# Optimization experiments

Measured on AMD Instinct MI355X. Metric: run time of the kernel, lower is better.

## Reference

```python
import jax, jax.numpy as jnp
import numpy as np

# Forest structure: T_TREES complete trees with branching BR and edge-depth DEPTH.
# Node layout: level-major; within a level, tree-major, siblings consecutive, so the
# parent of the k-th node of level l is the (k // BR)-th node of level l-1.
T_TREES, BR, DEPTH = 128, 2, 11
C, L, M, G = 8, 2, 256, 4  # hidden states, max outdegree, alphabet, n_gen
_sizes = [T_TREES * BR ** l for l in range(DEPTH + 1)]
_offs = np.concatenate([[0], np.cumsum(_sizes)])
DIM = int(_offs[-1])
LEVEL_NODES = [jnp.arange(int(_offs[l]), int(_offs[l + 1])) for l in range(DEPTH + 1)]
LEAVES = LEVEL_NODES[DEPTH]


def setup_inputs():
    key = jax.random.key(0)
    k = jax.random.split(key, 6)
    # batch id of node (level l, within-level idx i) is i // BR**l -> repeat pattern
    batch = jnp.concatenate([jnp.repeat(jnp.arange(T_TREES, dtype=jnp.int32), BR ** l)
                             for l in range(DEPTH + 1)])
    return {
        "lambda_A": jax.random.uniform(k[0], (C, C, L, G), dtype=jnp.float32),
        "lambda_B": jax.random.uniform(k[1], (C, M, G), dtype=jnp.float32),
        "lambda_Pi": jax.random.uniform(k[2], (C, L, G), dtype=jnp.float32),
        "lambda_SP": jax.random.uniform(k[3], (L, G), dtype=jnp.float32),
        "pos": jax.random.randint(k[4], (DIM,), 0, L, dtype=jnp.int32),
        "x": jax.random.randint(k[5], (DIM,), 0, M, dtype=jnp.int32),
        "batch": batch,
    }


def reference(lambda_A, lambda_B, lambda_Pi, lambda_SP, pos, x, batch):
    # Faithful ReversedUpwardDownward.forward ('bu' mode) of HiddenTreeMarkovModel.
    A = jax.nn.softmax(lambda_A, axis=0)    # (C,C,L,G): column-stochastic over parent state
    Bm = jax.nn.softmax(lambda_B, axis=1)   # (C,M,G): emission
    Pi = jax.nn.softmax(lambda_Pi, axis=0)  # (C,L,G): leaf prior per position
    SP = jax.nn.softmax(lambda_SP, axis=0)  # (L,G): switching-parent weights

    beta = jnp.zeros((DIM, C, G), lambda_A.dtype)
    ll = jnp.zeros((DIM, G), lambda_A.dtype)

    # leaves
    beta_lv = (Pi[:, pos[LEAVES]] * Bm[:, x[LEAVES]]).transpose(1, 0, 2)  # (nl,C,G)
    nu = beta_lv.sum(1)                                                   # (nl,G)
    beta = beta.at[LEAVES].set(beta_lv / nu[:, None])
    ll = ll.at[LEAVES].set(jnp.log(nu))

    # bottom-up level recursion
    for l in range(DEPTH, 0, -1):
        ch, pa = LEVEL_NODES[l], LEVEL_NODES[l - 1]
        pos_ch = pos[ch]                                   # (n,)
        # t_beta_ch[n,c,g] = SP[pos_ch] * sum_d A[c,d,pos_ch,g] * beta[ch][d,g]
        msgs = jnp.einsum('cdpg,ndg->ncpg', A, beta[ch])   # (n,C,L,G); avoids (n,C,C,G)
        sel = jax.nn.one_hot(pos_ch, L, dtype=msgs.dtype)  # (n,L)
        t_beta_ch = SP[pos_ch][:, None, :] * jnp.einsum('ncpg,np->ncg', msgs, sel)
        # scatter-add to parents == exact sum over the BR consecutive siblings
        t_beta_pa = t_beta_ch.reshape(pa.shape[0], BR, C, G).sum(1)  # (npa,C,G)
        beta_pa = t_beta_pa * Bm[:, x[pa]].transpose(1, 0, 2)
        nu = beta_pa.sum(1)
        beta = beta.at[pa].set(beta_pa / nu[:, None])
        ll = ll.at[pa].set(jnp.log(nu))

    # per-tree total log-likelihood
    return jax.ops.segment_sum(ll, batch, num_segments=T_TREES)  # (T_TREES, G)
```

## Files before the change

kernel.cpp:

```cpp
#include <hip/hip_runtime.h>
#include <math.h>


#define NTHREADS 1024
#define NSTRIDE 17

__global__ __launch_bounds__(NTHREADS) void htmm_kernel(
    const float* __restrict__ lA,
    const float* __restrict__ lB,
    const float* __restrict__ lPi,
    const float* __restrict__ lSP,
    const int* __restrict__ pos,
    const int* __restrict__ xx,
    float* __restrict__ out)
{
    __shared__ float sBm[16 * 256];
    __shared__ float sA[256];
    __shared__ float sPi[32];
    __shared__ float sSP[4];
    __shared__ float sInv[16];
    __shared__ float buf0[512 * NSTRIDE];
    __shared__ float buf1[256 * NSTRIDE];
    __shared__ double sLL[2];

    const int tid = threadIdx.x;
    const int t  = blockIdx.x >> 1;
    const int g0 = (blockIdx.x & 1) << 1;

    if (tid < 2) sLL[tid] = 0.0;

#pragma unroll
    for (int k = 0; k < 4; ++k) {
        int idx = tid + k * NTHREADS;
        int c = idx >> 9, m = (idx >> 1) & 255, gi = idx & 1;
        sBm[((c << 1) | gi) * 256 + m] = expf(lB[c * 1024 + m * 4 + g0 + gi]);
    }
    __syncthreads();

    if (tid < 256) {
        int r = tid >> 4, seg = tid & 15;
        float s = 0.f;
#pragma unroll
        for (int i = 0; i < 16; ++i) s += sBm[r * 256 + seg * 16 + ((i + seg) & 15)];
#pragma unroll
        for (int o = 8; o >= 1; o >>= 1) s += __shfl_xor(s, o, 64);
        if (seg == 0) sInv[r] = 1.0f / s;
    } else if (tid >= 256 && tid < 288) {
        int w = tid - 256;
        int d = w >> 2, pp = (w >> 1) & 1, gi = w & 1;
        float e[8]; float s = 0.f;
#pragma unroll
        for (int c = 0; c < 8; ++c) { e[c] = expf(lA[c * 64 + d * 8 + pp * 4 + g0 + gi]); s += e[c]; }
        float inv = 1.f / s;
#pragma unroll
        for (int c = 0; c < 8; ++c) sA[(((pp << 1) | gi) * 8 + c) * 8 + d] = e[c] * inv;
    } else if (tid >= 288 && tid < 292) {
        int w = tid - 288; int pp = w >> 1, gi = w & 1;
        float e[8]; float s = 0.f;
#pragma unroll
        for (int c = 0; c < 8; ++c) { e[c] = expf(lPi[c * 8 + pp * 4 + g0 + gi]); s += e[c]; }
        float inv = 1.f / s;
#pragma unroll
        for (int c = 0; c < 8; ++c) sPi[((pp << 1) | gi) * 8 + c] = e[c] * inv;
    } else if (tid >= 292 && tid < 294) {
        int gi = tid - 292;
        float e0 = expf(lSP[g0 + gi]), e1 = expf(lSP[4 + g0 + gi]);
        float inv = 1.f / (e0 + e1);
        sSP[gi] = e0 * inv; sSP[2 + gi] = e1 * inv;
    }
    __syncthreads();

#pragma unroll
    for (int k = 0; k < 4; ++k) {
        int idx = tid + k * NTHREADS;
        sBm[idx] *= sInv[idx >> 8];
    }
    __syncthreads();

    float ll0 = 0.f, ll1 = 0.f;

    {
        const int j  = tid & 511;
        const int gi = tid >> 9;
        const int4 pv4 = *(const int4*)(pos + 262016 + t * 2048 + 4 * j);
        const int4 xv4 = *(const int4*)(xx  + 262016 + t * 2048 + 4 * j);
        const int2 pu2 = *(const int2*)(pos + 130944 + t * 1024 + 2 * j);
        const int2 xu2 = *(const int2*)(xx  + 130944 + t * 1024 + 2 * j);
        const int xq = xx[65408 + t * 512 + j];

        float llacc = 0.f;
        float tq[8] = {0,0,0,0,0,0,0,0};
#pragma unroll
        for (int u = 0; u < 2; ++u) {
            float tu[8] = {0,0,0,0,0,0,0,0};
#pragma unroll
            for (int v = 0; v < 2; ++v) {
                const int k = 2 * u + v;
                const int pv  = (k == 0) ? pv4.x : (k == 1) ? pv4.y : (k == 2) ? pv4.z : pv4.w;
                const int xvv = (k == 0) ? xv4.x : (k == 1) ? xv4.y : (k == 2) ? xv4.z : xv4.w;
                const float* Pip = &sPi[((pv << 1) | gi) << 3];
                float b[8]; float nu = 0.f;
#pragma unroll
                for (int c = 0; c < 8; ++c) {
                    b[c] = Pip[c] * sBm[((c << 1) | gi) * 256 + xvv];
                    nu += b[c];
                }
                llacc += logf(nu);
                const float scale = sSP[(pv << 1) | gi] / nu;
                const float* Ap = &sA[((pv << 1) | gi) << 6];
#pragma unroll
                for (int c = 0; c < 8; ++c) {
                    float s = 0.f;
#pragma unroll
                    for (int d = 0; d < 8; ++d) s += Ap[(c << 3) + d] * b[d];
                    tu[c] += scale * s;
                }
            }
            const int pu = u ? pu2.y : pu2.x;
            const int xu = u ? xu2.y : xu2.x;
            float bu[8]; float nuu = 0.f;
#pragma unroll
            for (int c = 0; c < 8; ++c) { bu[c] = tu[c] * sBm[((c << 1) | gi) * 256 + xu]; nuu += bu[c]; }
            llacc += logf(nuu);
            const float scale = sSP[(pu << 1) | gi] / nuu;
            const float* Ap = &sA[((pu << 1) | gi) << 6];
#pragma unroll
            for (int c = 0; c < 8; ++c) {
                float s = 0.f;
#pragma unroll
                for (int d = 0; d < 8; ++d) s += Ap[(c << 3) + d] * bu[d];
                tq[c] += scale * s;
            }
        }
        float bq[8]; float nuq = 0.f;
#pragma unroll
        for (int c = 0; c < 8; ++c) { bq[c] = tq[c] * sBm[((c << 1) | gi) * 256 + xq]; nuq += bq[c]; }
        llacc += logf(nuq);
        const float inv = 1.f / nuq;
#pragma unroll
        for (int c = 0; c < 8; ++c) buf0[j * NSTRIDE + (gi << 3) + c] = bq[c] * inv;

        if (gi == 0) ll0 += llacc; else ll1 += llacc;
    }
    __syncthreads();

    float* bin = buf0;
    float* bout = buf1;
    for (int l = 9; l >= 1; --l) {
        const int nP = 1 << (l - 1);
        const int nItems = nP << 1;
        const int chBase = 128 * ((1 << l) - 1) + t * (1 << l);
        const int paBase = 128 * (nP - 1) + t * nP;
        if (tid < nItems) {
            const int p  = tid & (nP - 1);
            const int gi = tid >> (l - 1);
            const int2 pch = *(const int2*)(pos + chBase + 2 * p);
            const int xpa = xx[paBase + p];
            float tp[8] = {0,0,0,0,0,0,0,0};
#pragma unroll
            for (int u = 0; u < 2; ++u) {
                const int pw = u ? pch.y : pch.x;
                const float* bip = &bin[(2 * p + u) * NSTRIDE + (gi << 3)];
                float b[8];
#pragma unroll
                for (int d = 0; d < 8; ++d) b[d] = bip[d];
                const float scale = sSP[(pw << 1) | gi];
                const float* Ap = &sA[((pw << 1) | gi) << 6];
#pragma unroll
                for (int c = 0; c < 8; ++c) {
                    float s = 0.f;
#pragma unroll
                    for (int d = 0; d < 8; ++d) s += Ap[(c << 3) + d] * b[d];
                    tp[c] += scale * s;
                }
            }
            float bpv[8]; float nu = 0.f;
#pragma unroll
            for (int c = 0; c < 8; ++c) { bpv[c] = tp[c] * sBm[((c << 1) | gi) * 256 + xpa]; nu += bpv[c]; }
            const float llv = logf(nu);
            const float inv = 1.f / nu;
#pragma unroll
            for (int c = 0; c < 8; ++c) bout[p * NSTRIDE + (gi << 3) + c] = bpv[c] * inv;
            if (gi == 0) ll0 += llv; else ll1 += llv;
        }
        __syncthreads();
        float* tmpp = bin; bin = bout; bout = tmpp;
    }

    float r0 = ll0, r1 = ll1;
#pragma unroll
    for (int o = 32; o >= 1; o >>= 1) {
        r0 += __shfl_xor(r0, o, 64);
        r1 += __shfl_xor(r1, o, 64);
    }
    if ((tid & 63) == 0) {
        atomicAdd(&sLL[0], (double)r0);
        atomicAdd(&sLL[1], (double)r1);
    }
    __syncthreads();
    if (tid < 2) out[(t << 2) + g0 + tid] = (float)sLL[tid];
}

extern "C" void kernel_launch(void* const* d_in, const int* in_sizes, int n_in,
                              void* d_out, int out_size, void* d_ws, size_t ws_size,
                              hipStream_t stream) {
    const float* lA  = (const float*)d_in[0];
    const float* lB  = (const float*)d_in[1];
    const float* lPi = (const float*)d_in[2];
    const float* lSP = (const float*)d_in[3];
    const int*   pos = (const int*)d_in[4];
    const int*   xv  = (const int*)d_in[5];
    float* out = (float*)d_out;
    htmm_kernel<<<256, NTHREADS, 0, stream>>>(lA, lB, lPi, lSP, pos, xv, out);
}
```

Before: 94.02 us.

## Cache A/Pi/SP in registers, transpose emission table, use log2 accumulation

Transposes the emission table in shared memory to a [g][m][c] layout so each node's 8-state emission vector is fetched with two float4 loads instead of eight strided reads. Both position variants of the transition matrix, the leaf prior and the switching weights are preloaded into registers. Every node then computes both matvecs and selects by position, which removes data-dependent LDS indexing at the cost of double the FMAs and 128+ extra registers. Logs are accumulated with fast log2 and converted once at the end, and the upper-level work is remapped so both g-halves run in the same lanes. The heavy register use risks spilling at 1024 threads.

```diff
diff --git a/kernel.cpp b/kernel.cpp
--- a/kernel.cpp
+++ b/kernel.cpp
@@ -14,9 +14,9 @@
     const int* __restrict__ xx,
     float* __restrict__ out)
 {
-    __shared__ float sBm[16 * 256];
-    __shared__ float sA[256];
-    __shared__ float sPi[32];
+    __shared__ __align__(16) float sBm[2 * 256 * 8];
+    __shared__ __align__(16) float sA[256];
+    __shared__ __align__(16) float sPi[32];
     __shared__ float sSP[4];
     __shared__ float sInv[16];
     __shared__ float buf0[512 * NSTRIDE];
@@ -31,64 +31,106 @@
 
 #pragma unroll
     for (int k = 0; k < 4; ++k) {
-        int idx = tid + k * NTHREADS;
-        int c = idx >> 9, m = (idx >> 1) & 255, gi = idx & 1;
-        sBm[((c << 1) | gi) * 256 + m] = expf(lB[c * 1024 + m * 4 + g0 + gi]);
+        int w = tid + k * NTHREADS;
+        int gg = w >> 11, m = (w >> 3) & 255, c = w & 7;
+        sBm[w] = expf(lB[c * 1024 + m * 4 + g0 + gg]);
     }
     __syncthreads();
 
     if (tid < 256) {
         int r = tid >> 4, seg = tid & 15;
+        int gg = r >> 3, c = r & 7;
         float s = 0.f;
 #pragma unroll
-        for (int i = 0; i < 16; ++i) s += sBm[r * 256 + seg * 16 + ((i + seg) & 15)];
+        for (int i = 0; i < 16; ++i)
+            s += sBm[(gg << 11) + ((seg * 16 + i) << 3) + c];
 #pragma unroll
         for (int o = 8; o >= 1; o >>= 1) s += __shfl_xor(s, o, 64);
         if (seg == 0) sInv[r] = 1.0f / s;
     } else if (tid >= 256 && tid < 288) {
         int w = tid - 256;
-        int d = w >> 2, pp = (w >> 1) & 1, gi = w & 1;
+        int d = w >> 2, pp = (w >> 1) & 1, gg = w & 1;
         float e[8]; float s = 0.f;
 #pragma unroll
-        for (int c = 0; c < 8; ++c) { e[c] = expf(lA[c * 64 + d * 8 + pp * 4 + g0 + gi]); s += e[c]; }
+        for (int c = 0; c < 8; ++c) { e[c] = expf(lA[c * 64 + d * 8 + pp * 4 + g0 + gg]); s += e[c]; }
         float inv = 1.f / s;
 #pragma unroll
-        for (int c = 0; c < 8; ++c) sA[(((pp << 1) | gi) * 8 + c) * 8 + d] = e[c] * inv;
+        for (int c = 0; c < 8; ++c) sA[(((pp << 1) | gg) * 8 + c) * 8 + d] = e[c] * inv;
     } else if (tid >= 288 && tid < 292) {
-        int w = tid - 288; int pp = w >> 1, gi = w & 1;
+        int w = tid - 288; int pp = w >> 1, gg = w & 1;
         float e[8]; float s = 0.f;
 #pragma unroll
-        for (int c = 0; c < 8; ++c) { e[c] = expf(lPi[c * 8 + pp * 4 + g0 + gi]); s += e[c]; }
+        for (int c = 0; c < 8; ++c) { e[c] = expf(lPi[c * 8 + pp * 4 + g0 + gg]); s += e[c]; }
         float inv = 1.f / s;
 #pragma unroll
-        for (int c = 0; c < 8; ++c) sPi[((pp << 1) | gi) * 8 + c] = e[c] * inv;
+        for (int c = 0; c < 8; ++c) sPi[((pp << 1) | gg) * 8 + c] = e[c] * inv;
     } else if (tid >= 292 && tid < 294) {
-        int gi = tid - 292;
-        float e0 = expf(lSP[g0 + gi]), e1 = expf(lSP[4 + g0 + gi]);
+        int gg = tid - 292;
+        float e0 = expf(lSP[g0 + gg]), e1 = expf(lSP[4 + g0 + gg]);
         float inv = 1.f / (e0 + e1);
-        sSP[gi] = e0 * inv; sSP[2 + gi] = e1 * inv;
+        sSP[gg] = e0 * inv; sSP[2 + gg] = e1 * inv;
     }
     __syncthreads();
 
 #pragma unroll
     for (int k = 0; k < 4; ++k) {
-        int idx = tid + k * NTHREADS;
-        sBm[idx] *= sInv[idx >> 8];
-    }
-    __syncthreads();
-
-    float ll0 = 0.f, ll1 = 0.f;
-
+        int w = tid + k * NTHREADS;
+        sBm[w] *= sInv[((w >> 11) << 3) + (w & 7)];
+    }
+    __syncthreads();
+
+    const int gi = tid >> 9;
+    const int j  = tid & 511;
+
+    float A0r[64], A1r[64];
     {
-        const int j  = tid & 511;
-        const int gi = tid >> 9;
+        const float4* a0 = (const float4*)(sA + (gi << 6));
+        const float4* a1 = (const float4*)(sA + ((2 + gi) << 6));
+#pragma unroll
+        for (int q = 0; q < 16; ++q) {
+            float4 v0 = a0[q];
+            A0r[4 * q + 0] = v0.x; A0r[4 * q + 1] = v0.y; A0r[4 * q + 2] = v0.z; A0r[4 * q + 3] = v0.w;
+            float4 v1 = a1[q];
+            A1r[4 * q + 0] = v1.x; A1r[4 * q + 1] = v1.y; A1r[4 * q + 2] = v1.z; A1r[4 * q + 3] = v1.w;
+        }
+    }
+    float Pi0r[8], Pi1r[8];
+#pragma unroll
+    for (int c = 0; c < 8; ++c) { Pi0r[c] = sPi[(gi << 3) + c]; Pi1r[c] = sPi[((2 + gi) << 3) + c]; }
+    const float SP0 = sSP[gi], SP1 = sSP[2 + gi];
+
+    float llacc = 0.f;
+
+    auto matvec_acc = [&](const float (&b)[8], int pv, float scale, float (&acc)[8]) {
+        float s0[8], s1[8];
+#pragma unroll
+        for (int c = 0; c < 8; ++c) { s0[c] = 0.f; s1[c] = 0.f; }
+#pragma unroll
+        for (int c = 0; c < 8; ++c) {
+#pragma unroll
+            for (int d = 0; d < 8; ++d) {
+                s0[c] += A0r[(c << 3) + d] * b[d];
+                s1[c] += A1r[(c << 3) + d] * b[d];
+            }
+        }
+#pragma unroll
+        for (int c = 0; c < 8; ++c) acc[c] += scale * (pv ? s1[c] : s0[c]);
+    };
+
+    auto bm_gather = [&](int xv, float (&bm)[8]) {
+        const float4 v0 = *(const float4*)(sBm + (gi << 11) + (xv << 3));
+        const float4 v1 = *(const float4*)(sBm + (gi << 11) + (xv << 3) + 4);
+        bm[0] = v0.x; bm[1] = v0.y; bm[2] = v0.z; bm[3] = v0.w;
+        bm[4] = v1.x; bm[5] = v1.y; bm[6] = v1.z; bm[7] = v1.w;
+    };
+
+    {
         const int4 pv4 = *(const int4*)(pos + 262016 + t * 2048 + 4 * j);
         const int4 xv4 = *(const int4*)(xx  + 262016 + t * 2048 + 4 * j);
         const int2 pu2 = *(const int2*)(pos + 130944 + t * 1024 + 2 * j);
         const int2 xu2 = *(const int2*)(xx  + 130944 + t * 1024 + 2 * j);
         const int xq = xx[65408 + t * 512 + j];
 
-        float llacc = 0.f;
         float tq[8] = {0,0,0,0,0,0,0,0};
 #pragma unroll
         for (int u = 0; u < 2; ++u) {
@@ -98,49 +140,35 @@
                 const int k = 2 * u + v;
                 const int pv  = (k == 0) ? pv4.x : (k == 1) ? pv4.y : (k == 2) ? pv4.z : pv4.w;
                 const int xvv = (k == 0) ? xv4.x : (k == 1) ? xv4.y : (k == 2) ? xv4.z : xv4.w;
-                const float* Pip = &sPi[((pv << 1) | gi) << 3];
+                float bm[8]; bm_gather(xvv, bm);
                 float b[8]; float nu = 0.f;
 #pragma unroll
                 for (int c = 0; c < 8; ++c) {
-                    b[c] = Pip[c] * sBm[((c << 1) | gi) * 256 + xvv];
+                    b[c] = (pv ? Pi1r[c] : Pi0r[c]) * bm[c];
                     nu += b[c];
                 }
-                llacc += logf(nu);
-                const float scale = sSP[(pv << 1) | gi] / nu;
-                const float* Ap = &sA[((pv << 1) | gi) << 6];
-#pragma unroll
-                for (int c = 0; c < 8; ++c) {
-                    float s = 0.f;
-#pragma unroll
-                    for (int d = 0; d < 8; ++d) s += Ap[(c << 3) + d] * b[d];
-                    tu[c] += scale * s;
-                }
+                llacc += __log2f(nu);
+                const float scale = (pv ? SP1 : SP0) / nu;
+                matvec_acc(b, pv, scale, tu);
             }
             const int pu = u ? pu2.y : pu2.x;
             const int xu = u ? xu2.y : xu2.x;
+            float bm[8]; bm_gather(xu, bm);
             float bu[8]; float nuu = 0.f;
 #pragma unroll
-            for (int c = 0; c < 8; ++c) { bu[c] = tu[c] * sBm[((c << 1) | gi) * 256 + xu]; nuu += bu[c]; }
-            llacc += logf(nuu);
-            const float scale = sSP[(pu << 1) | gi] / nuu;
-            const float* Ap = &sA[((pu << 1) | gi) << 6];
-#pragma unroll
-            for (int c = 0; c < 8; ++c) {
-                float s = 0.f;
-#pragma unroll
-                for (int d = 0; d < 8; ++d) s += Ap[(c << 3) + d] * bu[d];
-                tq[c] += scale * s;
-            }
-        }
+            for (int c = 0; c < 8; ++c) { bu[c] = tu[c] * bm[c]; nuu += bu[c]; }
+            llacc += __log2f(nuu);
+            const float scale = (pu ? SP1 : SP0) / nuu;
+            matvec_acc(bu, pu, scale, tq);
+        }
+        float bm[8]; bm_gather(xq, bm);
         float bq[8]; float nuq = 0.f;
 #pragma unroll
-        for (int c = 0; c < 8; ++c) { bq[c] = tq[c] * sBm[((c << 1) | gi) * 256 + xq]; nuq += bq[c]; }
-        llacc += logf(nuq);
+        for (int c = 0; c < 8; ++c) { bq[c] = tq[c] * bm[c]; nuq += bq[c]; }
+        llacc += __log2f(nuq);
         const float inv = 1.f / nuq;
 #pragma unroll
         for (int c = 0; c < 8; ++c) buf0[j * NSTRIDE + (gi << 3) + c] = bq[c] * inv;
-
-        if (gi == 0) ll0 += llacc; else ll1 += llacc;
     }
     __syncthreads();
 
@@ -148,12 +176,10 @@
     float* bout = buf1;
     for (int l = 9; l >= 1; --l) {
         const int nP = 1 << (l - 1);
-        const int nItems = nP << 1;
         const int chBase = 128 * ((1 << l) - 1) + t * (1 << l);
         const int paBase = 128 * (nP - 1) + t * nP;
-        if (tid < nItems) {
-            const int p  = tid & (nP - 1);
-            const int gi = tid >> (l - 1);
+        if (j < nP) {
+            const int p = j;
             const int2 pch = *(const int2*)(pos + chBase + 2 * p);
             const int xpa = xx[paBase + p];
             float tp[8] = {0,0,0,0,0,0,0,0};
@@ -164,39 +190,25 @@
                 float b[8];
 #pragma unroll
                 for (int d = 0; d < 8; ++d) b[d] = bip[d];
-                const float scale = sSP[(pw << 1) | gi];
-                const float* Ap = &sA[((pw << 1) | gi) << 6];
-#pragma unroll
-                for (int c = 0; c < 8; ++c) {
-                    float s = 0.f;
-#pragma unroll
-                    for (int d = 0; d < 8; ++d) s += Ap[(c << 3) + d] * b[d];
-                    tp[c] += scale * s;
-                }
+                matvec_acc(b, pw, pw ? SP1 : SP0, tp);
             }
+            float bm[8]; bm_gather(xpa, bm);
             float bpv[8]; float nu = 0.f;
 #pragma unroll
-            for (int c = 0; c < 8; ++c) { bpv[c] = tp[c] * sBm[((c << 1) | gi) * 256 + xpa]; nu += bpv[c]; }
-            const float llv = logf(nu);
+            for (int c = 0; c < 8; ++c) { bpv[c] = tp[c] * bm[c]; nu += bpv[c]; }
+            llacc += __log2f(nu);
             const float inv = 1.f / nu;
 #pragma unroll
             for (int c = 0; c < 8; ++c) bout[p * NSTRIDE + (gi << 3) + c] = bpv[c] * inv;
-            if (gi == 0) ll0 += llv; else ll1 += llv;
         }
         __syncthreads();
         float* tmpp = bin; bin = bout; bout = tmpp;
     }
 
-    float r0 = ll0, r1 = ll1;
-#pragma unroll
-    for (int o = 32; o >= 1; o >>= 1) {
-        r0 += __shfl_xor(r0, o, 64);
-        r1 += __shfl_xor(r1, o, 64);
-    }
-    if ((tid & 63) == 0) {
-        atomicAdd(&sLL[0], (double)r0);
-        atomicAdd(&sLL[1], (double)r1);
-    }
+    float llf = llacc * 0.69314718055994530942f;
+#pragma unroll
+    for (int o = 32; o >= 1; o >>= 1) llf += __shfl_xor(llf, o, 64);
+    if ((tid & 63) == 0) atomicAdd(&sLL[gi], (double)llf);
     __syncthreads();
     if (tid < 2) out[(t << 2) + g0 + tid] = (float)sLL[tid];
 }
```

Result: slower. 140.0 us (+48.9%).
